# Kernel optimization log

Measured on AMD Instinct MI355X. Metric: run time of the kernel, lower is better.

Reference implementation:

```python
import jax, jax.numpy as jnp
import numpy as np

LIMIT = 7.0      # self.m.limit
ACT_ALPHA = 1.702  # self.m.alpha (GLU sigmoid slope)
R = 8
LORA_ALPHA = 16.0
SCALING = LORA_ALPHA / R
E, H, F = 8, 2048, 1024
D = 2 * F
B, S, K = 2, 1024, 4


def setup_inputs() -> dict:
    key = jax.random.key(0)
    ks = jax.random.split(key, 12)
    w = 0.02  # realistic weight scale
    return {
        "hidden_states": jax.random.normal(ks[0], (B, S, H), jnp.float32),
        "routing_weights": jax.random.uniform(ks[1], (B * S, K), jnp.float32),
        "gate_up_proj": jax.random.normal(ks[2], (E, H, D), jnp.float32) * w,
        "gate_up_proj_bias": jax.random.normal(ks[3], (E, D), jnp.float32) * w,
        "down_proj": jax.random.normal(ks[4], (E, F, H), jnp.float32) * w,
        "down_proj_bias": jax.random.normal(ks[5], (E, H), jnp.float32) * w,
        "lora_gate_up_A": jax.random.normal(ks[6], (E, H, R), jnp.float32) * w,
        "lora_gate_up_B": jax.random.normal(ks[7], (E, R, D), jnp.float32) * w,
        "lora_down_A": jax.random.normal(ks[8], (E, F, R), jnp.float32) * w,
        "lora_down_B": jax.random.normal(ks[9], (E, R, H), jnp.float32) * w,
        "router_indices": jax.random.randint(ks[10], (B * S, K), 0, E, jnp.int64),
    }


def reference(hidden_states, routing_weights, gate_up_proj, gate_up_proj_bias,
              down_proj, down_proj_bias, lora_gate_up_A, lora_gate_up_B,
              lora_down_A, lora_down_B, router_indices):
    b, s, h = hidden_states.shape
    x = hidden_states.reshape(-1, h)  # [T,H]
    # Combined per-(expert,token) routing weight: sum over top-k slots that hit expert e.
    onehot = jax.nn.one_hot(router_indices, E, dtype=x.dtype)        # [T,K,E]
    w = jnp.einsum('tke,tk->et', onehot, routing_weights)            # [E,T]
    # gate_up projection with inline LoRA (per expert, all tokens; masked by w later)
    lora1 = jnp.einsum('etr,erd->etd', jnp.einsum('th,ehr->etr', x, lora_gate_up_A), lora_gate_up_B)
    gate_up = jnp.einsum('th,ehd->etd', x, gate_up_proj) + SCALING * lora1 + gate_up_proj_bias[:, None, :]
    gate = jnp.minimum(gate_up[..., ::2], LIMIT)                     # [E,T,F]
    up = jnp.clip(gate_up[..., 1::2], -LIMIT, LIMIT)
    glu = gate * jax.nn.sigmoid(gate * ACT_ALPHA)
    gated = (up + 1.0) * glu                                         # [E,T,F]
    # down projection with inline LoRA
    lora2 = jnp.einsum('etr,erh->eth', jnp.einsum('etf,efr->etr', gated, lora_down_A), lora_down_B)
    out = jnp.einsum('etf,efh->eth', gated, down_proj) + SCALING * lora2 + down_proj_bias[:, None, :]
    # scatter-combine: weight each expert output and sum over experts
    next_states = jnp.einsum('et,eth->th', w, out)                   # [T,H]
    return next_states.reshape(b, s, h)
```

## Files before the change

kernel.cpp:

```cpp
#include <hip/hip_runtime.h>
#include <stdint.h>


typedef short bf16x8 __attribute__((ext_vector_type(8)));
typedef float f32x4 __attribute__((ext_vector_type(4)));

__device__ __forceinline__ short bf16r(float f) {
  uint32_t u = __float_as_uint(f);
  u += 0x7fffu + ((u >> 16) & 1u);
  return (short)(u >> 16);
}

__device__ __forceinline__ float bf16f(short s) {
  uint32_t u = ((uint32_t)(uint16_t)s) << 16;
  return __uint_as_float(u);
}

__device__ __forceinline__ void load_lds16(const void* g, void* l) {
  __builtin_amdgcn_global_load_lds((const __attribute__((address_space(1))) void*)g,
                                   (__attribute__((address_space(3))) void*)l,
                                   16, 0, 0);
}

__global__ void k_route(const int* __restrict__ idx_raw, const float* __restrict__ rw,
                        float* __restrict__ w, int* __restrict__ cnt, int* __restrict__ list,
                        int* __restrict__ tok_nh, int* __restrict__ tok_pair) {
  __shared__ int s_nz;
  const int tid = threadIdx.x;
  if (tid == 0) s_nz = 0;
  __syncthreads();
  int found = 0;
  for (int i = tid; i < 4096; i += 256) found |= idx_raw[2 * i + 1];
  if (found) atomicOr(&s_nz, 1);
  __syncthreads();
  const bool is64 = (s_nz == 0);

  const int t = blockIdx.x * 256 + tid;
  int ek[4]; float rk[4];
#pragma unroll
  for (int k = 0; k < 4; k++) {
    ek[k] = is64 ? idx_raw[2 * (t * 4 + k)] : idx_raw[t * 4 + k];
    rk[k] = rw[t * 4 + k];
  }
  int j = 0;
#pragma unroll
  for (int e = 0; e < 8; e++) {
    float s = 0.f;
#pragma unroll
    for (int k = 0; k < 4; k++) s += (ek[k] == e) ? rk[k] : 0.f;
    w[e * 2048 + t] = s;
    if (s != 0.f) {
      int slot = atomicAdd(&cnt[e], 1);
      list[e * 2048 + slot] = t;
      tok_pair[t * 4 + j] = (e << 16) | slot;
      j++;
    }
  }
  tok_nh[t] = j;
}

__global__ void k_prefix(const int* __restrict__ cnt, int* __restrict__ offs,
                         int* __restrict__ wl) {
  if (threadIdx.x == 0 && blockIdx.x == 0) {
    int s = 0; int nb[8];
    for (int e = 0; e < 8; e++) {
      offs[e] = s; s += cnt[e];
      nb[e] = (cnt[e] + 255) >> 8;
    }
    offs[8] = s;
    int p = 0;
    for (int j = 0; j < 64; j++)
      for (int e = 0; e < 8; e++)
        if (j < nb[e] * 8) wl[p++] = (e << 6) | j;
    offs[9] = p;
  }
}

__global__ void k_wprep(const float* __restrict__ W, const float* __restrict__ A,
                        const float* __restrict__ Bm, short* __restrict__ O,
                        int Kd, int Nd) {
  const int e = blockIdx.z;
  const float* We = W + (size_t)e * Kd * Nd;
  const float* Ae = A + (size_t)e * Kd * 8;
  const float* Be = Bm + (size_t)e * 8 * Nd;
  short* Oe = O + (size_t)e * Kd * Nd;
  __shared__ float tile[64][33];
  __shared__ float As[64][9];
  __shared__ float Bs[8][32];
  const int n0 = blockIdx.x * 32, k0 = blockIdx.y * 64;
  const int tx = threadIdx.x & 31, ty = threadIdx.x >> 5;
#pragma unroll
  for (int i = 0; i < 8; i++)
    tile[ty + 8 * i][tx] = We[(size_t)(k0 + ty + 8 * i) * Nd + n0 + tx];
  {
    int kk = threadIdx.x >> 3, r = threadIdx.x & 7;
    As[kk][r] = Ae[(size_t)(k0 + kk) * 8 + r];
    As[kk + 32][r] = Ae[(size_t)(k0 + kk + 32) * 8 + r];
  }
  {
    int rr = threadIdx.x >> 5, nn = threadIdx.x & 31;
    Bs[rr][nn] = Be[(size_t)rr * Nd + n0 + nn];
  }
  __syncthreads();
  const int kk2 = threadIdx.x & 63, ng = threadIdx.x >> 6;
#pragma unroll
  for (int i = 0; i < 8; i++) {
    int n = ng + 4 * i;
    float v = tile[kk2][n];
    float l = 0.f;
#pragma unroll
    for (int r = 0; r < 8; r++) l += As[kk2][r] * Bs[r][n];
    Oe[(size_t)(n0 + n) * Kd + k0 + kk2] = bf16r(v + 2.0f * l);
  }
}

__global__ void k_xconv(const float* __restrict__ x, short* __restrict__ xb) {
  const int i = (blockIdx.x * 256 + threadIdx.x) * 4;
  float4 v = *(const float4*)(x + i);
  short4 s;
  s.x = bf16r(v.x); s.y = bf16r(v.y); s.z = bf16r(v.z); s.w = bf16r(v.w);
  *(short4*)(xb + i) = s;
}


#define PH_SYNC() do { \
    asm volatile("s_barrier" ::: "memory"); \
    asm volatile("s_waitcnt lgkmcnt(0)" ::: "memory"); \
    __builtin_amdgcn_sched_barrier(0); \
    __builtin_amdgcn_s_setprio(1); } while (0)
#define PH_END() do { \
    __builtin_amdgcn_s_setprio(0); \
    asm volatile("s_barrier" ::: "memory"); } while (0)
#define PH_END_GATE() do { \
    __builtin_amdgcn_s_setprio(0); \
    asm volatile("s_waitcnt vmcnt(4)" ::: "memory"); \
    asm volatile("s_barrier" ::: "memory"); } while (0)

#define MM(AARR, BARR, MG, NG) \
  _Pragma("unroll") \
  for (int f_ = 0; f_ < 4; ++f_) \
    _Pragma("unroll") \
    for (int g_ = 0; g_ < 2; ++g_) \
      _Pragma("unroll") \
      for (int s_ = 0; s_ < 2; ++s_) \
        acc[(MG) + f_][(NG) + g_] = __builtin_amdgcn_mfma_f32_16x16x32_bf16( \
            AARR[f_][s_], BARR[g_][s_], acc[(MG) + f_][(NG) + g_], 0, 0, 0);

template <int KDIM, bool GATHER, bool GLU>
__global__ __launch_bounds__(512) void k_gemm8p(
    const short* __restrict__ Abuf, const short* __restrict__ Bbuf,
    const float* __restrict__ bias, const int* __restrict__ cnt,
    const int* __restrict__ offs, const int* __restrict__ wl,
    const int* __restrict__ list, short* __restrict__ outbuf) {
  constexpr int KT = KDIM / 64;
  constexpr int NIT = KT / 2;

  __shared__ __align__(16) short sA[2 * 256 * 64];
  __shared__ __align__(16) short sB[2 * 256 * 64];
  constexpr int SLOT = 256 * 64;
  constexpr int HALF = 128 * 64;

  const int tid = threadIdx.x;
  const int lane = tid & 63;
  const int wv = tid >> 6;
  const int wr = wv >> 2;
  const int wc = wv & 3;
  const int lm = lane & 15;
  const int quad = lane >> 4;

  const int srow = tid >> 3;
  const int scol = ((tid & 7) ^ (srow & 7)) * 8;

  const int rbA = (wr * 128 + lm) * 64;
  const int rbB = (wc * 64 + lm) * 64;
  const int c0 = ((0 + quad) ^ (lane & 7)) * 8;
  const int c1 = ((4 + quad) ^ (lane & 7)) * 8;

  const int nitems = offs[9];

  for (int item = blockIdx.x; item < nitems; item += 256) {
    const int wit = wl[item];
    const int e = wit >> 6;
    const int m0 = ((wit >> 3) & 7) * 256;
    const int n0 = (wit & 7) * 256;
    const int M = cnt[e];
    const int off_e = offs[e];
    const short* Bp = Bbuf + (size_t)e * 2048 * KDIM;

    uint32_t offA[4], offB[4];
#pragma unroll
    for (int j = 0; j < 4; ++j) {
      const int r = m0 + srow + 64 * j;
      const int rc = min(r, M - 1);
      if constexpr (GATHER) {
        offA[j] = (uint32_t)list[e * 2048 + rc] * (uint32_t)KDIM + (uint32_t)scol;
      } else {
        offA[j] = (uint32_t)(off_e + rc) * (uint32_t)KDIM + (uint32_t)scol;
      }
      offB[j] = (uint32_t)(n0 + srow + 64 * j) * (uint32_t)KDIM + (uint32_t)scol;
    }

    auto stageA = [&](int slot, int h, int kt) {
      short* d = sA + slot * SLOT + h * HALF + tid * 8;
      load_lds16(Abuf + offA[2 * h] + kt * 64, d);
      load_lds16(Abuf + offA[2 * h + 1] + kt * 64, d + 4096);
    };
    auto stageB = [&](int slot, int h, int kt) {
      short* d = sB + slot * SLOT + h * HALF + tid * 8;
      load_lds16(Bp + offB[2 * h] + kt * 64, d);
      load_lds16(Bp + offB[2 * h + 1] + kt * 64, d + 4096);
    };

    auto rdA = [&](int slot, int mg, bf16x8 (&a)[4][2]) {
#pragma unroll
      for (int f = 0; f < 4; ++f) {
        const short* p = sA + slot * SLOT + rbA + (mg + f) * 1024;
        a[f][0] = *(const bf16x8*)(p + c0);
        a[f][1] = *(const bf16x8*)(p + c1);
      }
    };
    auto rdB = [&](int slot, int ng, bf16x8 (&b)[2][2]) {
#pragma unroll
      for (int g = 0; g < 2; ++g) {
        const short* p = sB + slot * SLOT + rbB + (ng + g) * 1024;
        b[g][0] = *(const bf16x8*)(p + c0);
        b[g][1] = *(const bf16x8*)(p + c1);
      }
    };

    f32x4 acc[8][4];
#pragma unroll
    for (int i = 0; i < 8; ++i)
#pragma unroll
      for (int j = 0; j < 4; ++j) acc[i][j] = (f32x4){0.f, 0.f, 0.f, 0.f};

    stageB(0, 0, 0); stageB(0, 1, 0);
    stageA(0, 0, 0); stageA(0, 1, 0);
    {
      const int k1 = (1 < KT - 1) ? 1 : (KT - 1);
      stageB(1, 0, k1); stageB(1, 1, k1);
    }
    asm volatile("s_waitcnt vmcnt(4)" ::: "memory");
    asm volatile("s_barrier" ::: "memory");

    bf16x8 aLo[4][2], aHi[4][2], bLo[2][2], bHi[2][2];

#pragma unroll 1
    for (int it = 0; it < NIT; ++it) {
      const int tb = 2 * it + 1;
      const int tS0 = min(2 * it + 2, KT - 1);
      const int tS1 = min(2 * it + 3, KT - 1);
      rdA(0, 0, aLo); rdB(0, 0, bLo);
      stageA(1, 0, tb);
      PH_SYNC(); MM(aLo, bLo, 0, 0); PH_END();
      rdB(0, 2, bHi);
      stageA(1, 1, tb);
      PH_SYNC(); MM(aLo, bHi, 0, 2); PH_END();
      rdA(0, 4, aHi);
      stageB(0, 0, tS0);
      PH_SYNC(); MM(aHi, bLo, 4, 0); PH_END();
      stageB(0, 1, tS0);
      PH_SYNC(); MM(aHi, bHi, 4, 2); PH_END_GATE();
      rdA(1, 0, aLo); rdB(1, 0, bLo);
      stageA(0, 0, tS0);
      PH_SYNC(); MM(aLo, bLo, 0, 0); PH_END();
      rdB(1, 2, bHi);
      stageA(0, 1, tS0);
      PH_SYNC(); MM(aLo, bHi, 0, 2); PH_END();
      rdA(1, 4, aHi);
      stageB(1, 0, tS1);
      PH_SYNC(); MM(aHi, bLo, 4, 0); PH_END();
      stageB(1, 1, tS1);
      PH_SYNC(); MM(aHi, bHi, 4, 2); PH_END_GATE();
    }

    if constexpr (GLU) {
      const float* be = bias + e * 2048;
#pragma unroll
      for (int m = 0; m < 8; ++m) {
        const int rbase = m0 + wr * 128 + m * 16 + quad * 4;
#pragma unroll
        for (int g = 0; g < 4; ++g) {
          const int col = n0 + wc * 64 + g * 16 + lm;
          const float bb = be[col];
#pragma unroll
          for (int r = 0; r < 4; ++r) {
            const int slot = rbase + r;
            float val = acc[m][g][r] + bb;
            float other = __shfl_xor(val, 1);
            if (((lane & 1) == 0) && (slot < M)) {
              float gt = fminf(val, 7.f);
              float u = fminf(fmaxf(other, -7.f), 7.f);
              float glu = gt / (1.f + __expf(-1.702f * gt));
              outbuf[(size_t)(off_e + slot) * 1024 + (col >> 1)] = bf16r((u + 1.f) * glu);
            }
          }
        }
      }
    } else {
#pragma unroll
      for (int m = 0; m < 8; ++m) {
#pragma unroll
        for (int r = 0; r < 4; ++r) {
          const int slot = m0 + wr * 128 + m * 16 + quad * 4 + r;
          if (slot >= M) continue;
          short* prow = outbuf + (size_t)(off_e + slot) * 2048;
#pragma unroll
          for (int g = 0; g < 4; ++g) {
            const int h = n0 + wc * 64 + g * 16 + lm;
            prow[h] = bf16r(acc[m][g][r]);
          }
        }
      }
    }
  }
}

__global__ __launch_bounds__(256) void k_combine(
    const short* __restrict__ pairbuf, const float* __restrict__ bias2,
    const float* __restrict__ wbuf, const int* __restrict__ offs,
    const int* __restrict__ tok_nh, const int* __restrict__ tok_pair,
    float* __restrict__ out) {
  const int t = blockIdx.x;
  const int h0 = threadIdx.x * 8;
  const int nh = tok_nh[t];
  float acc[8];
#pragma unroll
  for (int i = 0; i < 8; i++) acc[i] = 0.f;
  for (int j = 0; j < nh; j++) {
    const int p = tok_pair[t * 4 + j];
    const int e = p >> 16, slot = p & 0xffff;
    const float wt = wbuf[e * 2048 + t];
    const bf16x8 v = *(const bf16x8*)(pairbuf + (size_t)(offs[e] + slot) * 2048 + h0);
    const float4 bA = *(const float4*)(bias2 + e * 2048 + h0);
    const float4 bB = *(const float4*)(bias2 + e * 2048 + h0 + 4);
    acc[0] += wt * (bf16f(v[0]) + bA.x);
    acc[1] += wt * (bf16f(v[1]) + bA.y);
    acc[2] += wt * (bf16f(v[2]) + bA.z);
    acc[3] += wt * (bf16f(v[3]) + bA.w);
    acc[4] += wt * (bf16f(v[4]) + bB.x);
    acc[5] += wt * (bf16f(v[5]) + bB.y);
    acc[6] += wt * (bf16f(v[6]) + bB.z);
    acc[7] += wt * (bf16f(v[7]) + bB.w);
  }
  float4 oA = {acc[0], acc[1], acc[2], acc[3]};
  float4 oB = {acc[4], acc[5], acc[6], acc[7]};
  *(float4*)(out + (size_t)t * 2048 + h0) = oA;
  *(float4*)(out + (size_t)t * 2048 + h0 + 4) = oB;
}

extern "C" void kernel_launch(void* const* d_in, const int* in_sizes, int n_in,
                              void* d_out, int out_size, void* d_ws, size_t ws_size,
                              hipStream_t stream) {
  const float* x   = (const float*)d_in[0];
  const float* rw  = (const float*)d_in[1];
  const float* w1  = (const float*)d_in[2];
  const float* b1  = (const float*)d_in[3];
  const float* w2  = (const float*)d_in[4];
  const float* b2  = (const float*)d_in[5];
  const float* a1  = (const float*)d_in[6];
  const float* lb1 = (const float*)d_in[7];
  const float* a2  = (const float*)d_in[8];
  const float* lb2 = (const float*)d_in[9];
  const int* idx   = (const int*)d_in[10];
  float* out = (float*)d_out;

  char* ws = (char*)d_ws;
  int* cnt     = (int*)(ws);
  int* offs    = (int*)(ws + 64);
  int* tok_nh  = (int*)(ws + 128);
  int* wl      = (int*)(ws + 8320);
  float* wbuf  = (float*)(ws + 16384);
  int* list    = (int*)(ws + 81920);
  int* tok_pair= (int*)(ws + 147456);
  short* Xb    = (short*)(ws + (1ull << 20));
  short* gated = (short*)(ws + 9437184ull);
  short* W2T   = (short*)(ws + 26214400ull);
  short* W1T   = (short*)(ws + 59768832ull);
  short* pairbuf = (short*)(ws + 59768832ull);

  hipMemsetAsync(cnt, 0, 64, stream);

  k_route<<<dim3(8), dim3(256), 0, stream>>>(idx, rw, wbuf, cnt, list, tok_nh, tok_pair);
  k_prefix<<<dim3(1), dim3(64), 0, stream>>>(cnt, offs, wl);
  k_wprep<<<dim3(64, 32, 8), dim3(256), 0, stream>>>(w1, a1, lb1, W1T, 2048, 2048);
  k_wprep<<<dim3(64, 16, 8), dim3(256), 0, stream>>>(w2, a2, lb2, W2T, 1024, 2048);
  k_xconv<<<dim3(4096), dim3(256), 0, stream>>>(x, Xb);
  k_gemm8p<2048, true, true><<<dim3(256), dim3(512), 0, stream>>>(
      Xb, W1T, b1, cnt, offs, wl, list, gated);
  k_gemm8p<1024, false, false><<<dim3(256), dim3(512), 0, stream>>>(
      gated, W2T, nullptr, cnt, offs, wl, nullptr, pairbuf);
  k_combine<<<dim3(2048), dim3(256), 0, stream>>>(pairbuf, b2, wbuf, offs, tok_nh, tok_pair, out);
}
```

Before: 440.1 us.

## Simplify GEMM k-loop pipeline, vectorize weight prep, parallelize worklist build

The GEMM main loop drops the eight-phase schedule, which had a barrier around every MFMA group. It now runs a per-k-tile loop that issues all LDS reads up front, then two MFMA halves with one barrier between them. The LoRA weight-merge kernel now uses float4 global loads and 16-byte bf16 stores instead of scalar accesses. The worklist is built by 512 threads in parallel, with -1 marking empty slots that the GEMM skips instead of reading a compacted count. Fewer barriers should reduce sync stalls, but the coarser schedule may overlap global staging with compute less well.

After: 416.5 us. 1.06x faster.

```diff
diff --git a/kernel.cpp b/kernel.cpp
--- a/kernel.cpp
+++ b/kernel.cpp
@@ -61,19 +61,18 @@
 
 __global__ void k_prefix(const int* __restrict__ cnt, int* __restrict__ offs,
                          int* __restrict__ wl) {
-  if (threadIdx.x == 0 && blockIdx.x == 0) {
-    int s = 0; int nb[8];
-    for (int e = 0; e < 8; e++) {
-      offs[e] = s; s += cnt[e];
-      nb[e] = (cnt[e] + 255) >> 8;
-    }
+  const int tid = threadIdx.x;
+  __shared__ int sc[8];
+  if (tid < 8) sc[tid] = cnt[tid];
+  __syncthreads();
+  if (tid == 0) {
+    int s = 0;
+    for (int e = 0; e < 8; e++) { offs[e] = s; s += sc[e]; }
     offs[8] = s;
-    int p = 0;
-    for (int j = 0; j < 64; j++)
-      for (int e = 0; e < 8; e++)
-        if (j < nb[e] * 8) wl[p++] = (e << 6) | j;
-    offs[9] = p;
-  }
+  }
+  const int j = tid >> 3, e = tid & 7;
+  const int nb = (sc[e] + 255) >> 8;
+  wl[tid] = (j < nb * 8) ? ((e << 6) | j) : -1;
 }
 
 __global__ void k_wprep(const float* __restrict__ W, const float* __restrict__ A,
@@ -88,10 +87,18 @@
   __shared__ float As[64][9];
   __shared__ float Bs[8][32];
   const int n0 = blockIdx.x * 32, k0 = blockIdx.y * 64;
-  const int tx = threadIdx.x & 31, ty = threadIdx.x >> 5;
-#pragma unroll
-  for (int i = 0; i < 8; i++)
-    tile[ty + 8 * i][tx] = We[(size_t)(k0 + ty + 8 * i) * Nd + n0 + tx];
+  {
+    const int rr = threadIdx.x >> 3;
+    const int cc = (threadIdx.x & 7) * 4;
+#pragma unroll
+    for (int h = 0; h < 2; h++) {
+      float4 v = *(const float4*)(We + (size_t)(k0 + rr + 32 * h) * Nd + n0 + cc);
+      tile[rr + 32 * h][cc + 0] = v.x;
+      tile[rr + 32 * h][cc + 1] = v.y;
+      tile[rr + 32 * h][cc + 2] = v.z;
+      tile[rr + 32 * h][cc + 3] = v.w;
+    }
+  }
   {
     int kk = threadIdx.x >> 3, r = threadIdx.x & 7;
     As[kk][r] = Ae[(size_t)(k0 + kk) * 8 + r];
@@ -102,16 +109,22 @@
     Bs[rr][nn] = Be[(size_t)rr * Nd + n0 + nn];
   }
   __syncthreads();
-  const int kk2 = threadIdx.x & 63, ng = threadIdx.x >> 6;
+  const int n2 = threadIdx.x >> 3;
+  const int kg = (threadIdx.x & 7) * 8;
+  float bl[8];
+#pragma unroll
+  for (int r = 0; r < 8; r++) bl[r] = Bs[r][n2];
+  short ov[8];
 #pragma unroll
   for (int i = 0; i < 8; i++) {
-    int n = ng + 4 * i;
-    float v = tile[kk2][n];
+    const int k = kg + i;
+    float v = tile[k][n2];
     float l = 0.f;
 #pragma unroll
-    for (int r = 0; r < 8; r++) l += As[kk2][r] * Bs[r][n];
-    Oe[(size_t)(n0 + n) * Kd + k0 + kk2] = bf16r(v + 2.0f * l);
-  }
+    for (int r = 0; r < 8; r++) l += As[k][r] * bl[r];
+    ov[i] = bf16r(v + 2.0f * l);
+  }
+  *(bf16x8*)(Oe + (size_t)(n0 + n2) * Kd + k0 + kg) = *(bf16x8*)ov;
 }
 
 __global__ void k_xconv(const float* __restrict__ x, short* __restrict__ xb) {
@@ -123,37 +136,23 @@
 }
 
 
-#define PH_SYNC() do { \
-    asm volatile("s_barrier" ::: "memory"); \
-    asm volatile("s_waitcnt lgkmcnt(0)" ::: "memory"); \
-    __builtin_amdgcn_sched_barrier(0); \
-    __builtin_amdgcn_s_setprio(1); } while (0)
-#define PH_END() do { \
-    __builtin_amdgcn_s_setprio(0); \
-    asm volatile("s_barrier" ::: "memory"); } while (0)
-#define PH_END_GATE() do { \
-    __builtin_amdgcn_s_setprio(0); \
-    asm volatile("s_waitcnt vmcnt(4)" ::: "memory"); \
-    asm volatile("s_barrier" ::: "memory"); } while (0)
-
-#define MM(AARR, BARR, MG, NG) \
+#define MM_S(AARR, BARR, MG, NG) \
   _Pragma("unroll") \
-  for (int f_ = 0; f_ < 4; ++f_) \
+  for (int s_ = 0; s_ < 2; ++s_) \
     _Pragma("unroll") \
-    for (int g_ = 0; g_ < 2; ++g_) \
+    for (int f_ = 0; f_ < 4; ++f_) \
       _Pragma("unroll") \
-      for (int s_ = 0; s_ < 2; ++s_) \
+      for (int g_ = 0; g_ < 2; ++g_) \
         acc[(MG) + f_][(NG) + g_] = __builtin_amdgcn_mfma_f32_16x16x32_bf16( \
             AARR[f_][s_], BARR[g_][s_], acc[(MG) + f_][(NG) + g_], 0, 0, 0);
 
 template <int KDIM, bool GATHER, bool GLU>
-__global__ __launch_bounds__(512) void k_gemm8p(
+__global__ __launch_bounds__(512) void k_gemmG(
     const short* __restrict__ Abuf, const short* __restrict__ Bbuf,
     const float* __restrict__ bias, const int* __restrict__ cnt,
     const int* __restrict__ offs, const int* __restrict__ wl,
     const int* __restrict__ list, short* __restrict__ outbuf) {
   constexpr int KT = KDIM / 64;
-  constexpr int NIT = KT / 2;
 
   __shared__ __align__(16) short sA[2 * 256 * 64];
   __shared__ __align__(16) short sB[2 * 256 * 64];
@@ -176,10 +175,9 @@
   const int c0 = ((0 + quad) ^ (lane & 7)) * 8;
   const int c1 = ((4 + quad) ^ (lane & 7)) * 8;
 
-  const int nitems = offs[9];
-
-  for (int item = blockIdx.x; item < nitems; item += 256) {
+  for (int item = blockIdx.x; item < 512; item += 256) {
     const int wit = wl[item];
+    if (wit < 0) continue;
     const int e = wit >> 6;
     const int m0 = ((wit >> 3) & 7) * 256;
     const int n0 = (wit & 7) * 256;
@@ -234,10 +232,12 @@
 #pragma unroll
       for (int j = 0; j < 4; ++j) acc[i][j] = (f32x4){0.f, 0.f, 0.f, 0.f};
 
+    asm volatile("s_waitcnt vmcnt(0)" ::: "memory");
+
+    stageA(0, 0, 0); stageA(0, 1, 0);
     stageB(0, 0, 0); stageB(0, 1, 0);
-    stageA(0, 0, 0); stageA(0, 1, 0);
     {
-      const int k1 = (1 < KT - 1) ? 1 : (KT - 1);
+      const int k1 = (KT > 1) ? 1 : 0;
       stageB(1, 0, k1); stageB(1, 1, k1);
     }
     asm volatile("s_waitcnt vmcnt(4)" ::: "memory");
@@ -246,32 +246,27 @@
     bf16x8 aLo[4][2], aHi[4][2], bLo[2][2], bHi[2][2];
 
 #pragma unroll 1
-    for (int it = 0; it < NIT; ++it) {
-      const int tb = 2 * it + 1;
-      const int tS0 = min(2 * it + 2, KT - 1);
-      const int tS1 = min(2 * it + 3, KT - 1);
-      rdA(0, 0, aLo); rdB(0, 0, bLo);
-      stageA(1, 0, tb);
-      PH_SYNC(); MM(aLo, bLo, 0, 0); PH_END();
-      rdB(0, 2, bHi);
-      stageA(1, 1, tb);
-      PH_SYNC(); MM(aLo, bHi, 0, 2); PH_END();
-      rdA(0, 4, aHi);
-      stageB(0, 0, tS0);
-      PH_SYNC(); MM(aHi, bLo, 4, 0); PH_END();
-      stageB(0, 1, tS0);
-      PH_SYNC(); MM(aHi, bHi, 4, 2); PH_END_GATE();
-      rdA(1, 0, aLo); rdB(1, 0, bLo);
-      stageA(0, 0, tS0);
-      PH_SYNC(); MM(aLo, bLo, 0, 0); PH_END();
-      rdB(1, 2, bHi);
-      stageA(0, 1, tS0);
-      PH_SYNC(); MM(aLo, bHi, 0, 2); PH_END();
-      rdA(1, 4, aHi);
-      stageB(1, 0, tS1);
-      PH_SYNC(); MM(aHi, bLo, 4, 0); PH_END();
-      stageB(1, 1, tS1);
-      PH_SYNC(); MM(aHi, bHi, 4, 2); PH_END_GATE();
+    for (int t = 0; t < KT; ++t) {
+      const int slot = t & 1;
+      const int tA = min(t + 1, KT - 1);
+      const int tB = min(t + 2, KT - 1);
+      rdA(slot, 0, aLo);
+      rdB(slot, 0, bLo);
+      rdB(slot, 2, bHi);
+      rdA(slot, 4, aHi);
+      stageA(slot ^ 1, 0, tA); stageA(slot ^ 1, 1, tA);
+      __builtin_amdgcn_s_setprio(1);
+      MM_S(aLo, bLo, 0, 0);
+      MM_S(aLo, bHi, 0, 2);
+      __builtin_amdgcn_s_setprio(0);
+      asm volatile("s_barrier" ::: "memory");
+      stageB(slot, 0, tB); stageB(slot, 1, tB);
+      __builtin_amdgcn_s_setprio(1);
+      MM_S(aHi, bLo, 4, 0);
+      MM_S(aHi, bHi, 4, 2);
+      __builtin_amdgcn_s_setprio(0);
+      asm volatile("s_waitcnt vmcnt(4)" ::: "memory");
+      asm volatile("s_barrier" ::: "memory");
     }
 
     if constexpr (GLU) {
@@ -382,13 +377,13 @@
   hipMemsetAsync(cnt, 0, 64, stream);
 
   k_route<<<dim3(8), dim3(256), 0, stream>>>(idx, rw, wbuf, cnt, list, tok_nh, tok_pair);
-  k_prefix<<<dim3(1), dim3(64), 0, stream>>>(cnt, offs, wl);
+  k_prefix<<<dim3(1), dim3(512), 0, stream>>>(cnt, offs, wl);
   k_wprep<<<dim3(64, 32, 8), dim3(256), 0, stream>>>(w1, a1, lb1, W1T, 2048, 2048);
   k_wprep<<<dim3(64, 16, 8), dim3(256), 0, stream>>>(w2, a2, lb2, W2T, 1024, 2048);
   k_xconv<<<dim3(4096), dim3(256), 0, stream>>>(x, Xb);
-  k_gemm8p<2048, true, true><<<dim3(256), dim3(512), 0, stream>>>(
+  k_gemmG<2048, true, true><<<dim3(256), dim3(512), 0, stream>>>(
       Xb, W1T, b1, cnt, offs, wl, list, gated);
-  k_gemm8p<1024, false, false><<<dim3(256), dim3(512), 0, stream>>>(
+  k_gemmG<1024, false, false><<<dim3(256), dim3(512), 0, stream>>>(
       gated, W2T, nullptr, cnt, offs, wl, nullptr, pairbuf);
   k_combine<<<dim3(2048), dim3(256), 0, stream>>>(pairbuf, b2, wbuf, offs, tok_nh, tok_pair, out);
 }
```
